# Kernel tuning notes

Hardware: AMD Instinct MI355X
Metric: run time of the kernel (lower is better)

Reference implementation:

```python
import jax, jax.numpy as jnp
import numpy as np

NMS_THRESH = 0.7
N_PRE = 12000
N_POST = 2000
IMG_X, IMG_Y = 1333.0, 402.0
MIN_SIZE = 16.0
FEAT_X, FEAT_Y, N_ANCH = 83, 25, 9   # int(1333/16), int(402/16), 9 anchors/cell
A = FEAT_X * FEAT_Y * N_ANCH         # 18675 anchors
CHUNK = 600                          # N_PRE % CHUNK == 0 -> 20 scan steps


def _make_anchors():
    stride = 16.0
    scales = np.array([8.0, 16.0, 32.0])
    ratios = np.array([0.5, 1.0, 2.0])
    hs = (stride * scales[:, None] * np.sqrt(ratios)[None, :]).ravel()  # 9 heights
    ws = (stride * scales[:, None] / np.sqrt(ratios)[None, :]).ravel()  # 9 widths
    cx = (np.arange(FEAT_X, dtype=np.float64) + 0.5) * stride
    cy = (np.arange(FEAT_Y, dtype=np.float64) + 0.5) * stride
    cxg, cyg = np.meshgrid(cx, cy, indexing="ij")  # [83,25]
    cxg = cxg[:, :, None]
    cyg = cyg[:, :, None]
    boxes = np.stack([cxg - 0.5 * ws, cyg - 0.5 * hs,
                      cxg + 0.5 * ws, cyg + 0.5 * hs], axis=-1)  # [83,25,9,4]
    return boxes.reshape(-1, 4).astype(np.float32)


def setup_inputs() -> dict:
    key = jax.random.key(0)
    k1, k2 = jax.random.split(key)
    return {
        "anchor_boxes": jnp.asarray(_make_anchors()),                          # [A,4]
        "rpn_cls_score": jax.random.normal(k1, (1, A, 2), jnp.float32),        # [B,A,2]
        "rpn_bbox_pred": jax.random.normal(k2, (1, A, 4), jnp.float32) * 0.1,  # [B,A,4]
    }


def _decode(anchor_boxes, rpn_cls_score, rpn_bbox_pred):
    # anchor geometry (same conventions as original: y from col1/3, x from col0/2)
    h_a = anchor_boxes[:, 3] - anchor_boxes[:, 1]
    w_a = anchor_boxes[:, 2] - anchor_boxes[:, 0]
    cy_a = anchor_boxes[:, 1] + 0.5 * h_a
    cx_a = anchor_boxes[:, 0] + 0.5 * w_a
    dx = rpn_bbox_pred[..., 0]
    dy = rpn_bbox_pred[..., 1]
    dw = rpn_bbox_pred[..., 2]
    dh = rpn_bbox_pred[..., 3]
    cy = dy * h_a + cy_a
    cx = dx * w_a + cx_a
    h = jnp.exp(dh) * h_a
    w = jnp.exp(dw) * w_a
    # clip: x coords to image_size[0], y coords to image_size[1] (as in original)
    x1 = jnp.clip(cx - 0.5 * w, 0.0, IMG_X)
    x2 = jnp.clip(cx + 0.5 * w, 0.0, IMG_X)
    y1 = jnp.clip(cy - 0.5 * h, 0.0, IMG_Y)
    y2 = jnp.clip(cy + 0.5 * h, 0.0, IMG_Y)
    roi = jnp.stack([x1, y1, x2, y2], axis=-1)  # [B,A,4]
    valid = ((y2 - y1) >= MIN_SIZE) & ((x2 - x1) >= MIN_SIZE)  # [B,A]
    score = rpn_cls_score[..., 1]  # objectness = channel 1 of 2-class score
    return roi, score, valid


def _nms_per_image(roi, score, valid):
    # sort valid boxes by descending score, take top N_PRE
    score = jnp.where(valid, score, -jnp.inf)
    order = jnp.argsort(-score)[:N_PRE]
    boxes = roi[order]  # [N_PRE,4]
    x1, y1, x2, y2 = boxes[:, 0], boxes[:, 1], boxes[:, 2], boxes[:, 3]
    areas = (x2 - x1 + 1.0) * (y2 - y1 + 1.0)
    idx = jnp.arange(N_PRE)

    def chunk_step(mark, zs):
        def row(z):
            xx1 = jnp.maximum(x1[z], x1)
            yy1 = jnp.maximum(y1[z], y1)
            xx2 = jnp.minimum(x2[z], x2)
            yy2 = jnp.minimum(y2[z], y2)
            w = jnp.maximum(0.0, xx2 - xx1 + 1.0)
            h = jnp.maximum(0.0, yy2 - yy1 + 1.0)
            inter = w * h
            ovr = inter / (areas[z] + areas - inter)
            over = ovr >= NMS_THRESH
            # faithful to original: np.where on the slice [z+1:] yields indices
            # RELATIVE to the slice, which are then used as absolute row indices.
            # So box k is deleted iff exists z with IoU(box z, box z+1+k) >= thresh.
            src = idx + z + 1
            contrib = jnp.where(src < N_PRE, over[jnp.minimum(src, N_PRE - 1)], False)
            return contrib & (z < N_PRE - 1)  # loop runs z in range(N_PRE-1)
        contribs = jax.vmap(row)(zs)  # [CHUNK, N_PRE]
        return mark | contribs.any(axis=0), None

    mark0 = jnp.zeros((N_PRE,), bool)
    mark, _ = jax.lax.scan(chunk_step, mark0, idx.reshape(-1, CHUNK))
    keep = ~mark
    # compact kept boxes to the front (stable), truncate to N_POST
    ord2 = jnp.argsort((~keep).astype(jnp.int32), stable=True)[:N_POST]
    kept = keep[ord2]
    out = jnp.where(kept[:, None], boxes[ord2], 0.0)  # zero-pad deleted slots
    return out, kept


def reference(anchor_boxes, rpn_cls_score, rpn_bbox_pred):
    roi, score, valid = _decode(anchor_boxes, rpn_cls_score, rpn_bbox_pred)
    rois, kept = jax.vmap(_nms_per_image)(roi, score, valid)
    return rois, kept  # [B,N_POST,4], [B,N_POST]
```

## Files before the change

### kernel.cpp

```cpp
#include <hip/hip_runtime.h>
#include <math.h>

#define A_TOT   18675
#define N_PRE   12000
#define N_POST  2000
#define IMG_X   1333.0f
#define IMG_Y   402.0f
#define MIN_SZ  16.0f
#define NMS_T   0.7f
#define NBUCK   4096

__global__ void decode_kernel(const float* __restrict__ anch,
                              const float* __restrict__ cls,
                              const float* __restrict__ pred,
                              float4* __restrict__ roi,
                              unsigned long long* __restrict__ key) {
    int i = blockIdx.x * blockDim.x + threadIdx.x;
    if (i >= A_TOT) return;

    float ax1 = anch[4*i+0], ay1 = anch[4*i+1], ax2 = anch[4*i+2], ay2 = anch[4*i+3];
    float h_a  = __fsub_rn(ay2, ay1);
    float w_a  = __fsub_rn(ax2, ax1);
    float cy_a = __fadd_rn(ay1, __fmul_rn(0.5f, h_a));
    float cx_a = __fadd_rn(ax1, __fmul_rn(0.5f, w_a));

    float dx = pred[4*i+0], dy = pred[4*i+1], dw = pred[4*i+2], dh = pred[4*i+3];

    float cy = __fadd_rn(__fmul_rn(dy, h_a), cy_a);
    float cx = __fadd_rn(__fmul_rn(dx, w_a), cx_a);
    float h  = __fmul_rn(expf(dh), h_a);
    float w  = __fmul_rn(expf(dw), w_a);

    float hw = __fmul_rn(0.5f, w);
    float hh = __fmul_rn(0.5f, h);
    float x1 = fminf(fmaxf(__fsub_rn(cx, hw), 0.0f), IMG_X);
    float x2 = fminf(fmaxf(__fadd_rn(cx, hw), 0.0f), IMG_X);
    float y1 = fminf(fmaxf(__fsub_rn(cy, hh), 0.0f), IMG_Y);
    float y2 = fminf(fmaxf(__fadd_rn(cy, hh), 0.0f), IMG_Y);

    bool valid = (__fsub_rn(y2, y1) >= MIN_SZ) && (__fsub_rn(x2, x1) >= MIN_SZ);

    roi[i] = make_float4(x1, y1, x2, y2);

    float s = valid ? cls[2*i+1] : -INFINITY;
    unsigned ub   = __float_as_uint(s);
    unsigned mask = ((unsigned)((int)ub >> 31)) | 0x80000000u;
    unsigned ord  = ub ^ mask;
    unsigned kd   = ~ord;
    key[i] = ((unsigned long long)kd << 32) | (unsigned)i;
}

__global__ __launch_bounds__(1024)
void sortprep_kernel(const unsigned long long* __restrict__ key,
                     unsigned long long* __restrict__ bkey,
                     unsigned* __restrict__ bstart,
                     unsigned* __restrict__ bcnt) {
    __shared__ unsigned cur[NBUCK];
    __shared__ unsigned wsum[16];
    const int t    = threadIdx.x;
    const int lane = t & 63;
    const int wv   = t >> 6;

#pragma unroll
    for (int e = 0; e < 4; ++e) cur[t + e * 1024] = 0u;
    __syncthreads();

    for (int j = t; j < A_TOT; j += 1024)
        atomicAdd(&cur[(unsigned)(key[j] >> 52)], 1u);
    __syncthreads();

    unsigned c0 = cur[4*t+0], c1 = cur[4*t+1], c2 = cur[4*t+2], c3 = cur[4*t+3];
    unsigned mysum = c0 + c1 + c2 + c3;

    unsigned incl = mysum;
#pragma unroll
    for (int off = 1; off < 64; off <<= 1) {
        unsigned v = __shfl_up(incl, off, 64);
        if (lane >= off) incl += v;
    }
    if (lane == 63) wsum[wv] = incl;
    __syncthreads();
    if (t == 0) {
        unsigned run = 0;
        for (int k = 0; k < 16; ++k) { unsigned v = wsum[k]; wsum[k] = run; run += v; }
    }
    __syncthreads();

    unsigned base = wsum[wv] + (incl - mysum);
    unsigned s0 = base, s1 = s0 + c0, s2 = s1 + c1, s3 = s2 + c2;

    ((uint4*)bstart)[t] = make_uint4(s0, s1, s2, s3);
    ((uint4*)bcnt)[t]   = make_uint4(c0, c1, c2, c3);

    cur[4*t+0] = s0; cur[4*t+1] = s1; cur[4*t+2] = s2; cur[4*t+3] = s3;
    __syncthreads();

    for (int j = t; j < A_TOT; j += 1024) {
        unsigned long long Ki = key[j];
        unsigned pos = atomicAdd(&cur[(unsigned)(Ki >> 52)], 1u);
        bkey[pos] = Ki;
    }
}

__global__ void rankscatter_kernel(const unsigned long long* __restrict__ bkey,
                                   const unsigned* __restrict__ bstart,
                                   const unsigned* __restrict__ bcnt,
                                   const float4* __restrict__ roi,
                                   float4* __restrict__ sboxes,
                                   float* __restrict__ sareas) {
    int g = blockIdx.x * blockDim.x + threadIdx.x;
    int p = g >> 6;
    int lane = g & 63;
    if (p >= A_TOT) return;

    unsigned long long Ki = bkey[p];
    unsigned b = (unsigned)(Ki >> 52);
    unsigned start = bstart[b];
    if (start >= N_PRE) return;
    unsigned cnt = bcnt[b];

    unsigned r = start;
    for (unsigned m = 0; m < cnt; m += 64) {
        unsigned mm = m + lane;
        bool lt = (mm < cnt) && (bkey[start + mm] < Ki);
        r += (unsigned)__popcll(__ballot(lt));
    }

    if (lane == 0 && r < N_PRE) {
        unsigned idx = (unsigned)Ki;
        float4 bx = roi[idx];
        sboxes[r] = bx;
        sareas[r] = __fmul_rn(__fadd_rn(__fsub_rn(bx.z, bx.x), 1.0f),
                              __fadd_rn(__fsub_rn(bx.w, bx.y), 1.0f));
    }
}

__global__ void nms_kernel(const float4* __restrict__ sboxes,
                           const float* __restrict__ sareas,
                           unsigned* __restrict__ mark) {
    int wid  = (blockIdx.x * blockDim.x + threadIdx.x) >> 6;
    int lane = threadIdx.x & 63;
    if (wid >= N_PRE) return;
    const int i      = wid;
    const int npairs = N_PRE - 1 - i;

    bool found = false;
    for (int base = 0; base < npairs; base += 64) {
        int z = base + lane;
        bool over = false;
        if (z < npairs) {
            float4 bz = sboxes[z];
            float4 bj = sboxes[z + i + 1];
            float az = sareas[z];
            float aj = sareas[z + i + 1];
            float xx1 = fmaxf(bz.x, bj.x);
            float yy1 = fmaxf(bz.y, bj.y);
            float xx2 = fminf(bz.z, bj.z);
            float yy2 = fminf(bz.w, bj.w);
            float w = fmaxf(0.0f, __fadd_rn(__fsub_rn(xx2, xx1), 1.0f));
            float h = fmaxf(0.0f, __fadd_rn(__fsub_rn(yy2, yy1), 1.0f));
            float inter = __fmul_rn(w, h);
            float denom = __fsub_rn(__fadd_rn(az, aj), inter);
            float ovr   = __fdiv_rn(inter, denom);
            over = (ovr >= NMS_T);
        }
        if (__any(over)) { found = true; break; }
    }
    if (lane == 0) mark[i] = found ? 1u : 0u;
}

__global__ __launch_bounds__(1024)
void output_kernel(const unsigned* __restrict__ mark,
                   const float4* __restrict__ sboxes,
                   float* __restrict__ out) {
    __shared__ int wsum[16];
    __shared__ int s_total;
    const int t    = threadIdx.x;
    const int lane = t & 63;
    const int wv   = t >> 6;
    const int E = 12;
    const int i0 = t * E;

    bool keep[E];
    int cnt = 0;
#pragma unroll
    for (int e = 0; e < E; ++e) {
        int i = i0 + e;
        bool k = (i < N_PRE) && (mark[i] == 0u);
        keep[e] = k;
        cnt += k ? 1 : 0;
    }

    int incl = cnt;
#pragma unroll
    for (int off = 1; off < 64; off <<= 1) {
        int v = __shfl_up(incl, off, 64);
        if (lane >= off) incl += v;
    }
    if (lane == 63) wsum[wv] = incl;
    __syncthreads();
    if (t == 0) {
        int run = 0;
        for (int k = 0; k < 16; ++k) { int v = wsum[k]; wsum[k] = run; run += v; }
        s_total = run;
    }
    __syncthreads();

    int base = wsum[wv] + (incl - cnt);
    const int total = s_total;

    int pos = base;
#pragma unroll
    for (int e = 0; e < E; ++e) {
        if (keep[e] && pos < N_POST) {
            float4 b = sboxes[i0 + e];
            out[4*pos+0] = b.x;
            out[4*pos+1] = b.y;
            out[4*pos+2] = b.z;
            out[4*pos+3] = b.w;
            out[4*N_POST + pos] = 1.0f;
        }
        pos += keep[e] ? 1 : 0;
    }
    for (int p = t; p < N_POST; p += 1024) {
        if (p >= total) {
            out[4*p+0] = 0.0f; out[4*p+1] = 0.0f;
            out[4*p+2] = 0.0f; out[4*p+3] = 0.0f;
            out[4*N_POST + p] = 0.0f;
        }
    }
}

extern "C" void kernel_launch(void* const* d_in, const int* in_sizes, int n_in,
                              void* d_out, int out_size, void* d_ws, size_t ws_size,
                              hipStream_t stream) {
    const float* anch = (const float*)d_in[0];
    const float* cls  = (const float*)d_in[1];
    const float* pred = (const float*)d_in[2];
    float* out = (float*)d_out;

    char* ws = (char*)d_ws;
    float4*             roi    = (float4*)(ws + 0);
    unsigned long long* key    = (unsigned long long*)(ws + 299008);
    unsigned long long* bkey   = (unsigned long long*)(ws + 448512);
    unsigned*           bstart = (unsigned*)(ws + 598016);
    unsigned*           bcnt   = (unsigned*)(ws + 614400);
    float4*             sboxes = (float4*)(ws + 630784);
    float*              sareas = (float*)(ws + 822784);
    unsigned*           mark   = (unsigned*)(ws + 870784);

    const int TB = 256;
    const int ablk = (A_TOT + TB - 1) / TB;
    const int rblk = (A_TOT * 64 + TB - 1) / TB;

    decode_kernel<<<ablk, TB, 0, stream>>>(anch, cls, pred, roi, key);
    sortprep_kernel<<<1, 1024, 0, stream>>>(key, bkey, bstart, bcnt);
    rankscatter_kernel<<<rblk, TB, 0, stream>>>(bkey, bstart, bcnt, roi, sboxes, sareas);
    nms_kernel<<<(N_PRE * 64) / TB, TB, 0, stream>>>(sboxes, sareas, mark);
    output_kernel<<<1, 1024, 0, stream>>>(mark, sboxes, out);
}
```

Baseline: 51.80 us.

## Parallelize bucket sort prep and output compaction across multiple blocks

Fuses decode with per-block bucket histograms, then replaces the single-block sort-prep with a multi-block scan and scatter that uses global atomic counters per bucket. The output compaction also moves from one block to twelve, with each block recomputing its prefix offset by scanning the mark array. The goal is to stop serialising the histogram/scatter and compaction stages on a single workgroup. In exchange, every block redundantly reduces all partial histograms and all marks, and the scatter order within a bucket is now nondeterministic, which rankscatter's comparison-based ranking tolerates.

```diff
diff --git a/kernel.cpp b/kernel.cpp
--- a/kernel.cpp
+++ b/kernel.cpp
@@ -9,67 +9,85 @@
 #define MIN_SZ  16.0f
 #define NMS_T   0.7f
 #define NBUCK   4096
-
-__global__ void decode_kernel(const float* __restrict__ anch,
-                              const float* __restrict__ cls,
-                              const float* __restrict__ pred,
-                              float4* __restrict__ roi,
-                              unsigned long long* __restrict__ key) {
-    int i = blockIdx.x * blockDim.x + threadIdx.x;
-    if (i >= A_TOT) return;
-
-    float ax1 = anch[4*i+0], ay1 = anch[4*i+1], ax2 = anch[4*i+2], ay2 = anch[4*i+3];
-    float h_a  = __fsub_rn(ay2, ay1);
-    float w_a  = __fsub_rn(ax2, ax1);
-    float cy_a = __fadd_rn(ay1, __fmul_rn(0.5f, h_a));
-    float cx_a = __fadd_rn(ax1, __fmul_rn(0.5f, w_a));
-
-    float dx = pred[4*i+0], dy = pred[4*i+1], dw = pred[4*i+2], dh = pred[4*i+3];
-
-    float cy = __fadd_rn(__fmul_rn(dy, h_a), cy_a);
-    float cx = __fadd_rn(__fmul_rn(dx, w_a), cx_a);
-    float h  = __fmul_rn(expf(dh), h_a);
-    float w  = __fmul_rn(expf(dw), w_a);
-
-    float hw = __fmul_rn(0.5f, w);
-    float hh = __fmul_rn(0.5f, h);
-    float x1 = fminf(fmaxf(__fsub_rn(cx, hw), 0.0f), IMG_X);
-    float x2 = fminf(fmaxf(__fadd_rn(cx, hw), 0.0f), IMG_X);
-    float y1 = fminf(fmaxf(__fsub_rn(cy, hh), 0.0f), IMG_Y);
-    float y2 = fminf(fmaxf(__fadd_rn(cy, hh), 0.0f), IMG_Y);
-
-    bool valid = (__fsub_rn(y2, y1) >= MIN_SZ) && (__fsub_rn(x2, x1) >= MIN_SZ);
-
-    roi[i] = make_float4(x1, y1, x2, y2);
-
-    float s = valid ? cls[2*i+1] : -INFINITY;
-    unsigned ub   = __float_as_uint(s);
-    unsigned mask = ((unsigned)((int)ub >> 31)) | 0x80000000u;
-    unsigned ord  = ub ^ mask;
-    unsigned kd   = ~ord;
-    key[i] = ((unsigned long long)kd << 32) | (unsigned)i;
-}
+#define NBLK1   19
 
 __global__ __launch_bounds__(1024)
-void sortprep_kernel(const unsigned long long* __restrict__ key,
-                     unsigned long long* __restrict__ bkey,
-                     unsigned* __restrict__ bstart,
-                     unsigned* __restrict__ bcnt) {
-    __shared__ unsigned cur[NBUCK];
+void decode_hist_kernel(const float* __restrict__ anch,
+                        const float* __restrict__ cls,
+                        const float* __restrict__ pred,
+                        float4* __restrict__ roi,
+                        unsigned long long* __restrict__ key,
+                        unsigned* __restrict__ phist,
+                        unsigned* __restrict__ gcnt) {
+    __shared__ unsigned lh[NBUCK];
+    const int t   = threadIdx.x;
+    const int blk = blockIdx.x;
+    const int g   = blk * 1024 + t;
+
+#pragma unroll
+    for (int e = 0; e < 4; ++e) lh[t + e * 1024] = 0u;
+    if (g < NBUCK) gcnt[g] = 0u;
+    __syncthreads();
+
+    if (g < A_TOT) {
+        float ax1 = anch[4*g+0], ay1 = anch[4*g+1], ax2 = anch[4*g+2], ay2 = anch[4*g+3];
+        float h_a  = __fsub_rn(ay2, ay1);
+        float w_a  = __fsub_rn(ax2, ax1);
+        float cy_a = __fadd_rn(ay1, __fmul_rn(0.5f, h_a));
+        float cx_a = __fadd_rn(ax1, __fmul_rn(0.5f, w_a));
+
+        float dx = pred[4*g+0], dy = pred[4*g+1], dw = pred[4*g+2], dh = pred[4*g+3];
+
+        float cy = __fadd_rn(__fmul_rn(dy, h_a), cy_a);
+        float cx = __fadd_rn(__fmul_rn(dx, w_a), cx_a);
+        float h  = __fmul_rn(expf(dh), h_a);
+        float w  = __fmul_rn(expf(dw), w_a);
+
+        float hw = __fmul_rn(0.5f, w);
+        float hh = __fmul_rn(0.5f, h);
+        float x1 = fminf(fmaxf(__fsub_rn(cx, hw), 0.0f), IMG_X);
+        float x2 = fminf(fmaxf(__fadd_rn(cx, hw), 0.0f), IMG_X);
+        float y1 = fminf(fmaxf(__fsub_rn(cy, hh), 0.0f), IMG_Y);
+        float y2 = fminf(fmaxf(__fadd_rn(cy, hh), 0.0f), IMG_Y);
+
+        bool valid = (__fsub_rn(y2, y1) >= MIN_SZ) && (__fsub_rn(x2, x1) >= MIN_SZ);
+
+        roi[g] = make_float4(x1, y1, x2, y2);
+
+        float s = valid ? cls[2*g+1] : -INFINITY;
+        unsigned ub   = __float_as_uint(s);
+        unsigned mask = ((unsigned)((int)ub >> 31)) | 0x80000000u;
+        unsigned ord  = ub ^ mask;
+        unsigned kd   = ~ord;
+        key[g] = ((unsigned long long)kd << 32) | (unsigned)g;
+        atomicAdd(&lh[kd >> 20], 1u);
+    }
+    __syncthreads();
+
+    ((uint4*)phist)[blk * 1024 + t] =
+        make_uint4(lh[4*t+0], lh[4*t+1], lh[4*t+2], lh[4*t+3]);
+}
+
+__global__ __launch_bounds__(1024)
+void scan_scatter_kernel(const unsigned long long* __restrict__ key,
+                         const unsigned* __restrict__ phist,
+                         unsigned* __restrict__ gcnt,
+                         unsigned* __restrict__ ghist,
+                         unsigned* __restrict__ gbstart,
+                         unsigned long long* __restrict__ bkey) {
+    __shared__ unsigned bs[NBUCK];
     __shared__ unsigned wsum[16];
     const int t    = threadIdx.x;
+    const int blk  = blockIdx.x;
     const int lane = t & 63;
     const int wv   = t >> 6;
 
-#pragma unroll
-    for (int e = 0; e < 4; ++e) cur[t + e * 1024] = 0u;
-    __syncthreads();
-
-    for (int j = t; j < A_TOT; j += 1024)
-        atomicAdd(&cur[(unsigned)(key[j] >> 52)], 1u);
-    __syncthreads();
-
-    unsigned c0 = cur[4*t+0], c1 = cur[4*t+1], c2 = cur[4*t+2], c3 = cur[4*t+3];
+    unsigned c0 = 0, c1 = 0, c2 = 0, c3 = 0;
+#pragma unroll
+    for (int k = 0; k < NBLK1; ++k) {
+        uint4 v = ((const uint4*)phist)[k * 1024 + t];
+        c0 += v.x; c1 += v.y; c2 += v.z; c3 += v.w;
+    }
     unsigned mysum = c0 + c1 + c2 + c3;
 
     unsigned incl = mysum;
@@ -88,23 +106,26 @@
 
     unsigned base = wsum[wv] + (incl - mysum);
     unsigned s0 = base, s1 = s0 + c0, s2 = s1 + c1, s3 = s2 + c2;
-
-    ((uint4*)bstart)[t] = make_uint4(s0, s1, s2, s3);
-    ((uint4*)bcnt)[t]   = make_uint4(c0, c1, c2, c3);
-
-    cur[4*t+0] = s0; cur[4*t+1] = s1; cur[4*t+2] = s2; cur[4*t+3] = s3;
-    __syncthreads();
-
-    for (int j = t; j < A_TOT; j += 1024) {
-        unsigned long long Ki = key[j];
-        unsigned pos = atomicAdd(&cur[(unsigned)(Ki >> 52)], 1u);
+    bs[4*t+0] = s0; bs[4*t+1] = s1; bs[4*t+2] = s2; bs[4*t+3] = s3;
+
+    if (blk == 0) {
+        ((uint4*)gbstart)[t] = make_uint4(s0, s1, s2, s3);
+        ((uint4*)ghist)[t]   = make_uint4(c0, c1, c2, c3);
+    }
+    __syncthreads();
+
+    int g = blk * 1024 + t;
+    if (g < A_TOT) {
+        unsigned long long Ki = key[g];
+        unsigned b = (unsigned)(Ki >> 52);
+        unsigned pos = bs[b] + atomicAdd(&gcnt[b], 1u);
         bkey[pos] = Ki;
     }
 }
 
 __global__ void rankscatter_kernel(const unsigned long long* __restrict__ bkey,
-                                   const unsigned* __restrict__ bstart,
-                                   const unsigned* __restrict__ bcnt,
+                                   const unsigned* __restrict__ gbstart,
+                                   const unsigned* __restrict__ ghist,
                                    const float4* __restrict__ roi,
                                    float4* __restrict__ sboxes,
                                    float* __restrict__ sareas) {
@@ -115,9 +136,9 @@
 
     unsigned long long Ki = bkey[p];
     unsigned b = (unsigned)(Ki >> 52);
-    unsigned start = bstart[b];
+    unsigned start = gbstart[b];
     if (start >= N_PRE) return;
-    unsigned cnt = bcnt[b];
+    unsigned cnt = ghist[b];
 
     unsigned r = start;
     for (unsigned m = 0; m < cnt; m += 64) {
@@ -173,61 +194,66 @@
 void output_kernel(const unsigned* __restrict__ mark,
                    const float4* __restrict__ sboxes,
                    float* __restrict__ out) {
-    __shared__ int wsum[16];
-    __shared__ int s_total;
+    __shared__ int wsA[16];
+    __shared__ int wsB[16];
+    __shared__ int wsS[16];
+    __shared__ int s_base, s_total;
     const int t    = threadIdx.x;
+    const int blk  = blockIdx.x;
     const int lane = t & 63;
     const int wv   = t >> 6;
-    const int E = 12;
-    const int i0 = t * E;
-
-    bool keep[E];
-    int cnt = 0;
-#pragma unroll
-    for (int e = 0; e < E; ++e) {
-        int i = i0 + e;
-        bool k = (i < N_PRE) && (mark[i] == 0u);
-        keep[e] = k;
-        cnt += k ? 1 : 0;
-    }
-
-    int incl = cnt;
+    const int limit = blk * 1024;
+
+    int sum_before = 0, sum_total = 0;
+    for (int j = t; j < N_PRE; j += 1024) {
+        int k = (mark[j] == 0u) ? 1 : 0;
+        sum_total += k;
+        if (j < limit) sum_before += k;
+    }
+#pragma unroll
+    for (int off = 32; off > 0; off >>= 1) {
+        sum_before += __shfl_xor(sum_before, off, 64);
+        sum_total  += __shfl_xor(sum_total,  off, 64);
+    }
+    if (lane == 0) { wsA[wv] = sum_before; wsB[wv] = sum_total; }
+    __syncthreads();
+    if (t == 0) {
+        int a = 0, b = 0;
+        for (int k = 0; k < 16; ++k) { a += wsA[k]; b += wsB[k]; }
+        s_base = a; s_total = b;
+    }
+    __syncthreads();
+
+    const int i = blk * 1024 + t;
+    int keep = (i < N_PRE) && (mark[i] == 0u);
+
+    int incl = keep;
 #pragma unroll
     for (int off = 1; off < 64; off <<= 1) {
         int v = __shfl_up(incl, off, 64);
         if (lane >= off) incl += v;
     }
-    if (lane == 63) wsum[wv] = incl;
+    if (lane == 63) wsS[wv] = incl;
     __syncthreads();
     if (t == 0) {
         int run = 0;
-        for (int k = 0; k < 16; ++k) { int v = wsum[k]; wsum[k] = run; run += v; }
-        s_total = run;
-    }
-    __syncthreads();
-
-    int base = wsum[wv] + (incl - cnt);
-    const int total = s_total;
-
-    int pos = base;
-#pragma unroll
-    for (int e = 0; e < E; ++e) {
-        if (keep[e] && pos < N_POST) {
-            float4 b = sboxes[i0 + e];
-            out[4*pos+0] = b.x;
-            out[4*pos+1] = b.y;
-            out[4*pos+2] = b.z;
-            out[4*pos+3] = b.w;
-            out[4*N_POST + pos] = 1.0f;
-        }
-        pos += keep[e] ? 1 : 0;
-    }
-    for (int p = t; p < N_POST; p += 1024) {
-        if (p >= total) {
-            out[4*p+0] = 0.0f; out[4*p+1] = 0.0f;
-            out[4*p+2] = 0.0f; out[4*p+3] = 0.0f;
-            out[4*N_POST + p] = 0.0f;
-        }
+        for (int k = 0; k < 16; ++k) { int v = wsS[k]; wsS[k] = run; run += v; }
+    }
+    __syncthreads();
+
+    int pos = s_base + wsS[wv] + (incl - keep);
+    if (keep && pos < N_POST) {
+        float4 b4 = sboxes[i];
+        out[4*pos+0] = b4.x;
+        out[4*pos+1] = b4.y;
+        out[4*pos+2] = b4.z;
+        out[4*pos+3] = b4.w;
+        out[4*N_POST + pos] = 1.0f;
+    }
+    if (i < N_POST && i >= s_total) {
+        out[4*i+0] = 0.0f; out[4*i+1] = 0.0f;
+        out[4*i+2] = 0.0f; out[4*i+3] = 0.0f;
+        out[4*N_POST + i] = 0.0f;
     }
 }
 
@@ -240,22 +266,23 @@
     float* out = (float*)d_out;
 
     char* ws = (char*)d_ws;
-    float4*             roi    = (float4*)(ws + 0);
-    unsigned long long* key    = (unsigned long long*)(ws + 299008);
-    unsigned long long* bkey   = (unsigned long long*)(ws + 448512);
-    unsigned*           bstart = (unsigned*)(ws + 598016);
-    unsigned*           bcnt   = (unsigned*)(ws + 614400);
-    float4*             sboxes = (float4*)(ws + 630784);
-    float*              sareas = (float*)(ws + 822784);
-    unsigned*           mark   = (unsigned*)(ws + 870784);
+    float4*             roi     = (float4*)(ws + 0);
+    unsigned long long* key     = (unsigned long long*)(ws + 299008);
+    unsigned*           phist   = (unsigned*)(ws + 448512);
+    unsigned*           gcnt    = (unsigned*)(ws + 759808);
+    unsigned*           ghist   = (unsigned*)(ws + 776192);
+    unsigned*           gbstart = (unsigned*)(ws + 792576);
+    unsigned long long* bkey    = (unsigned long long*)(ws + 808960);
+    float4*             sboxes  = (float4*)(ws + 958464);
+    float*              sareas  = (float*)(ws + 1150464);
+    unsigned*           mark    = (unsigned*)(ws + 1198464);
 
     const int TB = 256;
-    const int ablk = (A_TOT + TB - 1) / TB;
     const int rblk = (A_TOT * 64 + TB - 1) / TB;
 
-    decode_kernel<<<ablk, TB, 0, stream>>>(anch, cls, pred, roi, key);
-    sortprep_kernel<<<1, 1024, 0, stream>>>(key, bkey, bstart, bcnt);
-    rankscatter_kernel<<<rblk, TB, 0, stream>>>(bkey, bstart, bcnt, roi, sboxes, sareas);
+    decode_hist_kernel<<<NBLK1, 1024, 0, stream>>>(anch, cls, pred, roi, key, phist, gcnt);
+    scan_scatter_kernel<<<NBLK1, 1024, 0, stream>>>(key, phist, gcnt, ghist, gbstart, bkey);
+    rankscatter_kernel<<<rblk, TB, 0, stream>>>(bkey, gbstart, ghist, roi, sboxes, sareas);
     nms_kernel<<<(N_PRE * 64) / TB, TB, 0, stream>>>(sboxes, sareas, mark);
-    output_kernel<<<1, 1024, 0, stream>>>(mark, sboxes, out);
-}
+    output_kernel<<<12, 1024, 0, stream>>>(mark, sboxes, out);
+}
```

Result: slower. 57.96 us (+11.9%).
